# Kernel optimization log

Measured on AMD Instinct MI355X. Metric: run time of the kernel, lower is better.

## Reference

```python
import jax, jax.numpy as jnp
import numpy as np

K = 25          # kernel_size (number of B-spline control points)
DEGREE = 1      # open linear B-spline -> 2 nonzero basis weights per edge
N_NODES = 200000
N_EDGES = 6400000


def setup_inputs() -> dict:
    key = jax.random.key(0)
    k1, k2, k3, k4 = jax.random.split(key, 4)
    x = jax.random.normal(k1, (N_NODES, 2), dtype=jnp.float32)
    weight = jax.random.normal(k2, (K, 2, 1), dtype=jnp.float32)
    edges = jax.random.randint(k3, (2, N_EDGES), 0, N_NODES, dtype=jnp.int64)
    pseudo = jax.random.uniform(k4, (N_EDGES, 1), dtype=jnp.float32)
    return {"x": x, "weight": weight, "edges": edges, "pseudo": pseudo}


def reference(x, weight, edges, pseudo):
    # spline_conv with norm=True, no root_weight, no bias (forward only passes
    # x, edges, pseudo, weight, kernel_size=[25], is_open_spline=[1], degree, norm).
    row, col = edges[0], edges[1]   # messages gathered from col, scattered to row
    n = x.shape[0]

    # --- B-spline basis (open, degree 1, 1-D pseudo) ---
    p = pseudo[:, 0]                      # [E]
    v = p * (K - DEGREE)                  # [E], in [0, K-1)
    lo = jnp.floor(v)
    frac = v - lo                         # [E]
    i0 = jnp.clip(lo.astype(jnp.int32), 0, K - 1)       # [E]
    i1 = jnp.clip(i0 + 1, 0, K - 1)                     # [E]

    # --- gather + weighting: msg_e = sum_s basis[e,s] * x[col_e] @ W[idx[e,s]] ---
    xj = x[col]                                         # [E, 2]
    m0 = jnp.einsum('ef,efo->eo', xj, weight[i0])       # [E, 1]
    m1 = jnp.einsum('ef,efo->eo', xj, weight[i1])       # [E, 1]
    msg = (1.0 - frac)[:, None] * m0 + frac[:, None] * m1   # [E, 1]

    # --- scatter-add to target nodes ---
    out = jax.ops.segment_sum(msg, row, num_segments=n)     # [N, 1]

    # --- degree normalization (norm=True) ---
    deg = jax.ops.segment_sum(jnp.ones_like(p), row, num_segments=n)  # [N]
    out = out / jnp.clip(deg, 1.0, None)[:, None]
    return out
```

## Files before the change

### kernel.cpp

```cpp
#include <hip/hip_runtime.h>

#define KK 25
#define FP_SCALE 268435456.0f
#define FP_INV   (1.0f / 268435456.0f)

#define TPB 256
#define EPT 16
#define EPB (TPB * EPT)
#define WSHIFT 10
#define WNODE 1024
#define MAXBINS 256
#define CAP 36864

typedef unsigned long long u64;

__global__ void zero_counts(unsigned* __restrict__ p, int n) {
    int i = blockIdx.x * blockDim.x + threadIdx.x;
    if (i < n) p[i] = 0u;
}

__global__ __launch_bounds__(TPB, 8) void phase1(
    const float* __restrict__ x,
    const float* __restrict__ w,
    const int* __restrict__ row,
    const int* __restrict__ col,
    const float* __restrict__ pseudo,
    unsigned* __restrict__ bucket,
    unsigned* __restrict__ gcount,
    int n_edges)
{
    __shared__ float wsm[KK * 2];
    __shared__ unsigned bin_cnt[MAXBINS];
    __shared__ unsigned bin_start[MAXBINS];
    __shared__ unsigned bin_gbase[MAXBINS];
    __shared__ unsigned stage[EPB];

    const int tid = threadIdx.x;
    if (tid < KK * 2) wsm[tid] = w[tid];
    bin_cnt[tid] = 0u;
    __syncthreads();

    const long long base = (long long)blockIdx.x * EPB;
    const bool full = (base + EPB) <= (long long)n_edges;
    const int nloc = full ? EPB
                          : (int)(((long long)n_edges - base) > 0
                                      ? ((long long)n_edges - base) : 0LL);

    int rloc[EPT];
    if (full) {
        const int4* r4 = (const int4*)&row[base + (long long)tid * EPT];
        #pragma unroll
        for (int q = 0; q < EPT / 4; ++q) {
            int4 rr = r4[q];
            rloc[4 * q + 0] = rr.x; rloc[4 * q + 1] = rr.y;
            rloc[4 * q + 2] = rr.z; rloc[4 * q + 3] = rr.w;
        }
        #pragma unroll
        for (int k = 0; k < EPT; ++k)
            atomicAdd(&bin_cnt[rloc[k] >> WSHIFT], 1u);
    } else {
        for (int k = 0; k < EPT; ++k) {
            int i = tid * EPT + k;
            if (i < nloc) {
                int r = row[base + i];
                rloc[k] = r;
                atomicAdd(&bin_cnt[r >> WSHIFT], 1u);
            } else rloc[k] = -1;
        }
    }
    __syncthreads();

    unsigned v = bin_cnt[tid];
    bin_start[tid] = v;
    __syncthreads();
    for (int off = 1; off < MAXBINS; off <<= 1) {
        unsigned t = (tid >= off) ? bin_start[tid - off] : 0u;
        __syncthreads();
        bin_start[tid] += t;
        __syncthreads();
    }
    unsigned excl = bin_start[tid] - v;
    bin_start[tid] = excl;
    bin_cnt[tid]   = excl;
    bin_gbase[tid] = v ? atomicAdd(&gcount[tid], v) : 0u;
    __syncthreads();

    const float2* __restrict__ x2 = (const float2*)x;
    if (full) {
        const int4*   c4 = (const int4*)&col[base + (long long)tid * EPT];
        const float4* p4 = (const float4*)&pseudo[base + (long long)tid * EPT];
        #pragma unroll
        for (int q = 0; q < EPT / 4; ++q) {
            int4   cc = c4[q];
            float4 pp = p4[q];
            int   ca[4] = {cc.x, cc.y, cc.z, cc.w};
            float pa[4] = {pp.x, pp.y, pp.z, pp.w};
            #pragma unroll
            for (int j = 0; j < 4; ++j) {
                int   r  = rloc[4 * q + j];
                float vv = pa[j] * (float)(KK - 1);
                float lo = floorf(vv);
                float fr = vv - lo;
                int i0 = min(max((int)lo, 0), KK - 1);
                int i1 = min(i0 + 1, KK - 1);
                float2 xj = x2[ca[j]];
                float m0 = xj.x * wsm[2 * i0] + xj.y * wsm[2 * i0 + 1];
                float m1 = xj.x * wsm[2 * i1] + xj.y * wsm[2 * i1 + 1];
                float msg = (1.0f - fr) * m0 + fr * m1;
                unsigned ub = (__float_as_uint(msg) + 0x200u) & 0xFFFFFC00u;
                unsigned entry = ub | (unsigned)(r & (WNODE - 1));
                int bin = r >> WSHIFT;
                unsigned pos = atomicAdd(&bin_cnt[bin], 1u);
                stage[pos] = entry;
            }
        }
    } else {
        for (int k = 0; k < EPT; ++k) {
            int i = tid * EPT + k;
            if (i < nloc) {
                long long e = base + i;
                int r = rloc[k];
                int c = col[e];
                float p = pseudo[e];
                float vv = p * (float)(KK - 1);
                float lo = floorf(vv);
                float fr = vv - lo;
                int i0 = min(max((int)lo, 0), KK - 1);
                int i1 = min(i0 + 1, KK - 1);
                float2 xj = x2[c];
                float m0 = xj.x * wsm[2 * i0] + xj.y * wsm[2 * i0 + 1];
                float m1 = xj.x * wsm[2 * i1] + xj.y * wsm[2 * i1 + 1];
                float msg = (1.0f - fr) * m0 + fr * m1;
                unsigned ub = (__float_as_uint(msg) + 0x200u) & 0xFFFFFC00u;
                unsigned entry = ub | (unsigned)(r & (WNODE - 1));
                int bin = r >> WSHIFT;
                unsigned pos = atomicAdd(&bin_cnt[bin], 1u);
                stage[pos] = entry;
            }
        }
    }
    __syncthreads();

    for (int i = tid; i < nloc; i += TPB) {
        unsigned entry = stage[i];
        int b = 0;
        #pragma unroll
        for (int s = 128; s >= 1; s >>= 1) {
            int m = b + s;
            if (m < MAXBINS && (int)bin_start[m] <= i) b = m;
        }
        unsigned g = bin_gbase[b] + ((unsigned)i - bin_start[b]);
        if (g < CAP) bucket[(size_t)b * CAP + g] = entry;
    }
}

__global__ __launch_bounds__(1024) void phase2(
    const unsigned* __restrict__ bucket,
    const unsigned* __restrict__ gcount,
    float* __restrict__ out, int n_nodes)
{
    __shared__ u64 acc[WNODE];
    const int tid = threadIdx.x;
    const int bin = blockIdx.x;

    acc[tid] = 0ULL;
    __syncthreads();

    unsigned cnt = gcount[bin];
    if (cnt > CAP) cnt = CAP;
    const unsigned* __restrict__ bb = bucket + (size_t)bin * CAP;

    const unsigned nvec = cnt >> 2;
    const uint4* __restrict__ b4 = (const uint4*)bb;
    for (unsigned i = tid; i < nvec; i += 1024) {
        uint4 e4 = b4[i];
        unsigned ee[4] = {e4.x, e4.y, e4.z, e4.w};
        #pragma unroll
        for (int j = 0; j < 4; ++j) {
            unsigned e = ee[j];
            float msg = __uint_as_float(e & 0xFFFFFC00u);
            long long fx = (long long)llrintf(msg * FP_SCALE);
            atomicAdd(&acc[e & (WNODE - 1)], ((u64)fx << 16) | 1ULL);
        }
    }
    for (unsigned i = (nvec << 2) + tid; i < cnt; i += 1024) {
        unsigned e = bb[i];
        float msg = __uint_as_float(e & 0xFFFFFC00u);
        long long fx = (long long)llrintf(msg * FP_SCALE);
        atomicAdd(&acc[e & (WNODE - 1)], ((u64)fx << 16) | 1ULL);
    }
    __syncthreads();

    const int node = (bin << WSHIFT) + tid;
    if (node < n_nodes) {
        u64 t = acc[tid];
        int count = (int)(t & 0xFFFFULL);
        long long sf = ((long long)t) >> 16;
        float sum = (float)sf * FP_INV;
        out[node] = sum / (float)max(count, 1);
    }
}

__global__ void zero_acc(u64* __restrict__ p, int n) {
    int i = blockIdx.x * blockDim.x + threadIdx.x;
    if (i < n) p[i] = 0ULL;
}

__global__ void edge_kernel_flat(const float* __restrict__ x,
                                 const float* __restrict__ w,
                                 const int* __restrict__ row,
                                 const int* __restrict__ col,
                                 const float* __restrict__ pseudo,
                                 u64* __restrict__ acc,
                                 int n_edges) {
    __shared__ float wsm[KK * 2];
    if (threadIdx.x < KK * 2) wsm[threadIdx.x] = w[threadIdx.x];
    __syncthreads();

    const float2* __restrict__ x2 = (const float2*)x;
    int e = blockIdx.x * blockDim.x + threadIdx.x;
    if (e >= n_edges) return;

    int r = row[e];
    int c = col[e];
    float p = pseudo[e];
    float vv = p * (float)(KK - 1);
    float lo = floorf(vv);
    float fr = vv - lo;
    int i0 = min(max((int)lo, 0), KK - 1);
    int i1 = min(i0 + 1, KK - 1);
    float2 xj = x2[c];
    float m0 = xj.x * wsm[2 * i0] + xj.y * wsm[2 * i0 + 1];
    float m1 = xj.x * wsm[2 * i1] + xj.y * wsm[2 * i1 + 1];
    float msg = (1.0f - fr) * m0 + fr * m1;

    long long fx = (long long)llrintf(msg * FP_SCALE);
    atomicAdd(&acc[r], ((u64)fx << 16) + 1ULL);
}

__global__ void finalize_flat(const u64* __restrict__ acc,
                              float* __restrict__ out, int n) {
    int i = blockIdx.x * blockDim.x + threadIdx.x;
    if (i >= n) return;
    u64 t = acc[i];
    int count = (int)(t & 0xFFFFULL);
    long long sf = ((long long)t) >> 16;
    float sum = (float)sf * FP_INV;
    out[i] = sum / (float)max(count, 1);
}

extern "C" void kernel_launch(void* const* d_in, const int* in_sizes, int n_in,
                              void* d_out, int out_size, void* d_ws, size_t ws_size,
                              hipStream_t stream) {
    const float* x      = (const float*)d_in[0];
    const float* w      = (const float*)d_in[1];
    const int*   edges  = (const int*)d_in[2];
    const float* pseudo = (const float*)d_in[3];

    const int n_edges = in_sizes[3];
    const int n_nodes = out_size;

    const int* row = edges;
    const int* col = edges + n_edges;

    const int nbins = (n_nodes + WNODE - 1) >> WSHIFT;
    const size_t need = 4096 + (size_t)nbins * CAP * sizeof(unsigned);

    if (nbins <= MAXBINS && ws_size >= need) {
        unsigned* gcount = (unsigned*)d_ws;
        unsigned* bucket = (unsigned*)((char*)d_ws + 4096);

        zero_counts<<<1, MAXBINS, 0, stream>>>(gcount, MAXBINS);

        int blocks = (n_edges + EPB - 1) / EPB;
        phase1<<<blocks, TPB, 0, stream>>>(x, w, row, col, pseudo,
                                           bucket, gcount, n_edges);

        phase2<<<nbins, 1024, 0, stream>>>(bucket, gcount,
                                           (float*)d_out, n_nodes);
    } else {
        u64* acc = (u64*)d_ws;
        zero_acc<<<(n_nodes + 255) / 256, 256, 0, stream>>>(acc, n_nodes);
        int blocks = (n_edges + 255) / 256;
        edge_kernel_flat<<<blocks, 256, 0, stream>>>(x, w, row, col, pseudo,
                                                     acc, n_edges);
        finalize_flat<<<(n_nodes + 255) / 256, 256, 0, stream>>>(acc,
                                                                 (float*)d_out,
                                                                 n_nodes);
    }
}
```

Before: 179.8 us.

## Record per-edge bin rank in count pass, shuffle scan, per-bin copy-out

Phase 1 now keeps the rank returned by the first shared-memory atomic for each edge, packed with its bin and local node. The second atomic pass is no longer needed, because the staging position is bin_start plus that rank. The block-level prefix scan now uses wavefront shuffles instead of repeated shared-memory passes with barriers. The copy-out drops the per-entry binary search: each thread copies its own bin's contiguous run. In exchange, those global stores are strided across threads rather than coalesced, and work is unbalanced across threads, with some bins empty.

Measured after the change: 196.3 us. 9.2% more time.

```diff
diff --git a/kernel.cpp b/kernel.cpp
--- a/kernel.cpp
+++ b/kernel.cpp
@@ -33,6 +33,7 @@
     __shared__ unsigned bin_cnt[MAXBINS];
     __shared__ unsigned bin_start[MAXBINS];
     __shared__ unsigned bin_gbase[MAXBINS];
+    __shared__ unsigned wtot[4];
     __shared__ unsigned stage[EPB];
 
     const int tid = threadIdx.x;
@@ -46,9 +47,10 @@
                           : (int)(((long long)n_edges - base) > 0
                                       ? ((long long)n_edges - base) : 0LL);
 
-    int rloc[EPT];
+    unsigned pk[EPT];
     if (full) {
         const int4* r4 = (const int4*)&row[base + (long long)tid * EPT];
+        int rloc[EPT];
         #pragma unroll
         for (int q = 0; q < EPT / 4; ++q) {
             int4 rr = r4[q];
@@ -56,33 +58,45 @@
             rloc[4 * q + 2] = rr.z; rloc[4 * q + 3] = rr.w;
         }
         #pragma unroll
-        for (int k = 0; k < EPT; ++k)
-            atomicAdd(&bin_cnt[rloc[k] >> WSHIFT], 1u);
+        for (int k = 0; k < EPT; ++k) {
+            int r = rloc[k];
+            int bin = r >> WSHIFT;
+            unsigned rank = atomicAdd(&bin_cnt[bin], 1u);
+            pk[k] = ((unsigned)bin << 22) | (rank << 10)
+                  | (unsigned)(r & (WNODE - 1));
+        }
     } else {
         for (int k = 0; k < EPT; ++k) {
             int i = tid * EPT + k;
             if (i < nloc) {
                 int r = row[base + i];
-                rloc[k] = r;
-                atomicAdd(&bin_cnt[r >> WSHIFT], 1u);
-            } else rloc[k] = -1;
-        }
-    }
-    __syncthreads();
-
-    unsigned v = bin_cnt[tid];
-    bin_start[tid] = v;
-    __syncthreads();
-    for (int off = 1; off < MAXBINS; off <<= 1) {
-        unsigned t = (tid >= off) ? bin_start[tid - off] : 0u;
+                int bin = r >> WSHIFT;
+                unsigned rank = atomicAdd(&bin_cnt[bin], 1u);
+                pk[k] = ((unsigned)bin << 22) | (rank << 10)
+                      | (unsigned)(r & (WNODE - 1));
+            } else pk[k] = 0xFFFFFFFFu;
+        }
+    }
+    __syncthreads();
+
+    {
+        unsigned v = bin_cnt[tid];
+        unsigned incl = v;
+        #pragma unroll
+        for (int d = 1; d < 64; d <<= 1) {
+            unsigned t = __shfl_up(incl, d, 64);
+            if ((tid & 63) >= d) incl += t;
+        }
+        if ((tid & 63) == 63) wtot[tid >> 6] = incl;
         __syncthreads();
-        bin_start[tid] += t;
-        __syncthreads();
-    }
-    unsigned excl = bin_start[tid] - v;
-    bin_start[tid] = excl;
-    bin_cnt[tid]   = excl;
-    bin_gbase[tid] = v ? atomicAdd(&gcount[tid], v) : 0u;
+        unsigned off = 0;
+        const int wv = tid >> 6;
+        #pragma unroll
+        for (int ww = 0; ww < 4; ++ww)
+            if (ww < wv) off += wtot[ww];
+        bin_start[tid] = off + incl - v;
+        bin_gbase[tid] = v ? atomicAdd(&gcount[tid], v) : 0u;
+    }
     __syncthreads();
 
     const float2* __restrict__ x2 = (const float2*)x;
@@ -97,7 +111,7 @@
             float pa[4] = {pp.x, pp.y, pp.z, pp.w};
             #pragma unroll
             for (int j = 0; j < 4; ++j) {
-                int   r  = rloc[4 * q + j];
+                unsigned p = pk[4 * q + j];
                 float vv = pa[j] * (float)(KK - 1);
                 float lo = floorf(vv);
                 float fr = vv - lo;
@@ -108,9 +122,8 @@
                 float m1 = xj.x * wsm[2 * i1] + xj.y * wsm[2 * i1 + 1];
                 float msg = (1.0f - fr) * m0 + fr * m1;
                 unsigned ub = (__float_as_uint(msg) + 0x200u) & 0xFFFFFC00u;
-                unsigned entry = ub | (unsigned)(r & (WNODE - 1));
-                int bin = r >> WSHIFT;
-                unsigned pos = atomicAdd(&bin_cnt[bin], 1u);
+                unsigned entry = ub | (p & (WNODE - 1));
+                unsigned pos = bin_start[p >> 22] + ((p >> 10) & 0xFFFu);
                 stage[pos] = entry;
             }
         }
@@ -118,11 +131,11 @@
         for (int k = 0; k < EPT; ++k) {
             int i = tid * EPT + k;
             if (i < nloc) {
+                unsigned p = pk[k];
                 long long e = base + i;
-                int r = rloc[k];
                 int c = col[e];
-                float p = pseudo[e];
-                float vv = p * (float)(KK - 1);
+                float ps = pseudo[e];
+                float vv = ps * (float)(KK - 1);
                 float lo = floorf(vv);
                 float fr = vv - lo;
                 int i0 = min(max((int)lo, 0), KK - 1);
@@ -132,25 +145,23 @@
                 float m1 = xj.x * wsm[2 * i1] + xj.y * wsm[2 * i1 + 1];
                 float msg = (1.0f - fr) * m0 + fr * m1;
                 unsigned ub = (__float_as_uint(msg) + 0x200u) & 0xFFFFFC00u;
-                unsigned entry = ub | (unsigned)(r & (WNODE - 1));
-                int bin = r >> WSHIFT;
-                unsigned pos = atomicAdd(&bin_cnt[bin], 1u);
+                unsigned entry = ub | (p & (WNODE - 1));
+                unsigned pos = bin_start[p >> 22] + ((p >> 10) & 0xFFFu);
                 stage[pos] = entry;
             }
         }
     }
     __syncthreads();
 
-    for (int i = tid; i < nloc; i += TPB) {
-        unsigned entry = stage[i];
-        int b = 0;
-        #pragma unroll
-        for (int s = 128; s >= 1; s >>= 1) {
-            int m = b + s;
-            if (m < MAXBINS && (int)bin_start[m] <= i) b = m;
-        }
-        unsigned g = bin_gbase[b] + ((unsigned)i - bin_start[b]);
-        if (g < CAP) bucket[(size_t)b * CAP + g] = entry;
+    {
+        unsigned cnt = bin_cnt[tid];
+        unsigned st  = bin_start[tid];
+        unsigned gb  = bin_gbase[tid];
+        unsigned* __restrict__ dst = bucket + (size_t)tid * CAP;
+        for (unsigned j = 0; j < cnt; ++j) {
+            unsigned g = gb + j;
+            if (g < CAP) dst[g] = stage[st + j];
+        }
     }
 }
 
```
